# Optimization experiments

Hardware: AMD Instinct MI355X
Metric: run time of the kernel (lower is better)

## Reference

```python
import jax, jax.numpy as jnp
import numpy as np


def setup_inputs() -> dict:
    key = jax.random.key(0)
    k1, k2, k3, k4 = jax.random.split(key, 4)
    return {
        "src_feat1": jax.random.normal(k1, (4, 1024, 64, 64), dtype=jnp.float32),
        "tar_feat1": jax.random.normal(k2, (4, 1024, 64, 64), dtype=jnp.float32),
        "src_feat2": jax.random.normal(k3, (4, 2048, 32, 32), dtype=jnp.float32),
        "tar_feat2": jax.random.normal(k4, (4, 2048, 32, 32), dtype=jnp.float32),
    }


def _nn_concat(src, tar):
    # src: [B,C,H1,W1], tar: [B,C,H2,W2] -> [B,2C,H1,W1]
    B, C, H, W = src.shape
    s = src.reshape(B, C, -1).transpose(0, 2, 1)   # [B,N1,C]
    t = tar.reshape(B, C, -1).transpose(0, 2, 1)   # [B,N2,C]
    # squared euclidean distance (argmin of d^2 == argmin of d, sqrt monotonic)
    d2 = (
        jnp.sum(s * s, axis=-1, keepdims=True)      # [B,N1,1]
        + jnp.sum(t * t, axis=-1)[:, None, :]       # [B,1,N2]
        - 2.0 * jnp.einsum("bnc,bmc->bnm", s, t)    # [B,N1,N2]
    )
    idx = jnp.argmin(d2, axis=2)                    # [B,N1]
    nearest = jnp.take_along_axis(t, idx[..., None], axis=1)  # [B,N1,C]
    nearest = nearest.transpose(0, 2, 1).reshape(B, C, H, W)
    return jnp.concatenate([src, nearest], axis=1)


def reference(src_feat1, tar_feat1, src_feat2, tar_feat2):
    c1 = _nn_concat(src_feat1, tar_feat1)           # [B,2048,64,64]
    c2 = _nn_concat(src_feat2, tar_feat2)           # [B,4096,32,32]
    B, C2 = c2.shape[:2]
    H1, W1 = c1.shape[2], c1.shape[3]
    # F.interpolate(mode='bilinear', align_corners=False) == jax.image.resize 'linear'
    c2r = jax.image.resize(c2, (B, C2, H1, W1), method="linear")
    return jnp.concatenate([c1, c2r], axis=1)       # [B,6144,64,64]
```

## Files before the change

### kernel.cpp

```cpp
#include <hip/hip_runtime.h>
#include <cstdint>

using u8 = unsigned char;
using u64 = unsigned long long;

typedef _Float16 f16x8 __attribute__((ext_vector_type(8)));
typedef float f32x4 __attribute__((ext_vector_type(4)));
typedef unsigned short u16x8 __attribute__((ext_vector_type(8)));

__device__ __forceinline__ void gload16(const void* g, void* l) {
  __builtin_amdgcn_global_load_lds((const __attribute__((address_space(1))) void*)g,
                                   (__attribute__((address_space(3))) void*)l, 16, 0, 0);
}

#define VMCNT(N) asm volatile("s_waitcnt vmcnt(" #N ")" ::: "memory")

template <bool WITH_HN>
__global__ __launch_bounds__(256) void split_convert(const float* __restrict__ in,
                                                     _Float16* __restrict__ hi,
                                                     _Float16* __restrict__ lo,
                                                     float* __restrict__ hnp,
                                                     int C, int N) {
  const int n = blockIdx.y * 256 + threadIdx.x;
  const int c0 = blockIdx.x * 32;
  const int b = blockIdx.z;
  const float* inB = in + (size_t)b * C * N;
  f16x8 hv[4], lv[4];
  float ss = 0.f;
#pragma unroll
  for (int g = 0; g < 4; ++g)
#pragma unroll
    for (int e = 0; e < 8; ++e) {
      float x = inB[(size_t)(c0 + g * 8 + e) * N + n];
      _Float16 h = (_Float16)x;
      float r = (x - (float)h) * 4096.f;
      hv[g][e] = h;
      lv[g][e] = (_Float16)r;
      if (WITH_HN) ss = fmaf(x, x, ss);
    }
  _Float16* oh = hi + ((size_t)b * N + n) * C + c0;
  _Float16* ol = lo + ((size_t)b * N + n) * C + c0;
#pragma unroll
  for (int g = 0; g < 4; ++g) {
    *(f16x8*)(oh + g * 8) = hv[g];
    *(f16x8*)(ol + g * 8) = lv[g];
  }
  if (WITH_HN)
    hnp[((size_t)b * gridDim.x + blockIdx.x) * N + n] = ss;
}

__global__ __launch_bounds__(256) void hn_reduce(const float* __restrict__ hnp,
                                                 float* __restrict__ hn,
                                                 int NC, int N) {
  const int n = blockIdx.x * 256 + threadIdx.x;
  const int b = blockIdx.y;
  float acc = 0.f;
  for (int cc = 0; cc < NC; ++cc) acc += hnp[((size_t)b * NC + cc) * N + n];
  hn[(size_t)b * N + n] = 0.5f * acc;
}

#define MFMA_BLOCK(GI)                                                         \
  __builtin_amdgcn_s_barrier();                                                \
  asm volatile("s_waitcnt lgkmcnt(0)" ::: "memory");                           \
  __builtin_amdgcn_sched_barrier(0);                                           \
  __builtin_amdgcn_s_setprio(1);                                               \
  _Pragma("unroll") for (int i2 = 0; i2 < 4; ++i2)                             \
      _Pragma("unroll") for (int j = 0; j < NJ; ++j) acc[(GI)*4 + i2][j] =     \
      __builtin_amdgcn_mfma_f32_16x16x32_f16(av[i2], bv[j],                    \
                                             acc[(GI)*4 + i2][j], 0, 0, 0);    \
  __builtin_amdgcn_s_setprio(0);                                               \
  asm volatile("" ::: "memory");                                               \
  __builtin_amdgcn_s_barrier();

template <int MI, int NJ, int WCN, int NTH>
__global__ __launch_bounds__(NTH, 2) void nn_filter8(
    const u8* __restrict__ Ahi, const u8* __restrict__ Bhi,
    const float* __restrict__ hn, unsigned short* __restrict__ sc,
    int M, int N, int NT , int mBlocks, int nBlocks) {
  constexpr int BM = 2 * MI * 16;
  constexpr int G = MI / 4;
  constexpr int CHUNK_A = BM * 64;
  constexpr int CHUNK = 2 * CHUNK_A;
  __shared__ u8 smem[4 * CHUNK];

  const int tid = threadIdx.x;
  const int lane = tid & 63;
  const int wid = tid >> 6;
  const int wrow = wid / WCN;
  const int wcol = wid % WCN;
  const int lr = lane & 15, kh = lane >> 4;

  const int cpx = (int)gridDim.x >> 3;
  const int bid = (int)blockIdx.x;
  const int sbid = (bid & 7) * cpx + (bid >> 3);
  const int perB = mBlocks * nBlocks;
  const int b = sbid / perB;
  const int rr = sbid - b * perB;
  const int n1 = rr & 3;
  const int t2 = rr >> 2;
  const int mb = t2 % mBlocks;
  const int n2 = t2 / mBlocks;
  const int mbase = mb * BM;
  const int nbase = (n2 * 4 + n1) * BM;
  const size_t rstride = (size_t)NT * 128;

  const int r0 = (tid >> 6) * 16 + ((tid & 63) >> 2);
  const int sA = ((lane & 3) ^ (r0 >> 1)) & 3;
  const u8* aP0 = Ahi + ((size_t)b * M + mbase + r0) * rstride + sA * 16;
  const u8* aP1 = aP0 + (size_t)(NTH / 4) * rstride;
  const u8* bP0 = Bhi + ((size_t)b * N + nbase + r0) * rstride + sA * 16;
  const u8* bP1 = bP0 + (size_t)(NTH / 4) * rstride;

  auto STAGE = [&](int X, int h) {
    const size_t ko = (size_t)X * 128 + h * 64;
    u8* cb = smem + ((X & 1) * 2 + h) * CHUNK;
    gload16(aP0 + ko, cb + tid * 16);
    gload16(aP1 + ko, cb + NTH * 16 + tid * 16);
    gload16(bP0 + ko, cb + CHUNK_A + tid * 16);
    gload16(bP1 + ko, cb + CHUNK_A + NTH * 16 + tid * 16);
  };

  int a_off[MI], b_off[NJ];
#pragma unroll
  for (int i = 0; i < MI; ++i) {
    const int row = wrow * (MI * 16) + i * 16 + lr;
    a_off[i] = row * 64 + (((kh ^ (row >> 1)) & 3) << 4);
  }
#pragma unroll
  for (int j = 0; j < NJ; ++j) {
    const int row = wcol * (NJ * 16) + j * 16 + lr;
    b_off[j] = CHUNK_A + row * 64 + (((kh ^ (row >> 1)) & 3) << 4);
  }

  f32x4 acc[MI][NJ];
#pragma unroll
  for (int i = 0; i < MI; ++i)
#pragma unroll
    for (int j = 0; j < NJ; ++j) acc[i][j] = f32x4{0.f, 0.f, 0.f, 0.f};

  STAGE(0, 0);
  STAGE(0, 1);
  STAGE(1, 0);
  VMCNT(8);
  __builtin_amdgcn_s_barrier();

  for (int X = 0; X < NT; ++X) {
    const u8* cb0 = smem + ((X & 1) * 2) * CHUNK;
    const u8* cb1 = cb0 + CHUNK;
    f16x8 av[4], bv[NJ];

#pragma unroll
    for (int j = 0; j < NJ; ++j) bv[j] = *(const f16x8*)(cb0 + b_off[j]);
#pragma unroll
    for (int i2 = 0; i2 < 4; ++i2) av[i2] = *(const f16x8*)(cb0 + a_off[i2]);
    if (X + 1 < NT) STAGE(X + 1, 1);
    if (X + 1 < NT) { VMCNT(8); } else { VMCNT(0); }
    MFMA_BLOCK(0)

    if constexpr (G == 2) {
#pragma unroll
      for (int i2 = 0; i2 < 4; ++i2) av[i2] = *(const f16x8*)(cb0 + a_off[4 + i2]);
      MFMA_BLOCK(1)
    }

#pragma unroll
    for (int j = 0; j < NJ; ++j) bv[j] = *(const f16x8*)(cb1 + b_off[j]);
#pragma unroll
    for (int i2 = 0; i2 < 4; ++i2) av[i2] = *(const f16x8*)(cb1 + a_off[i2]);
    if (X + 2 < NT) STAGE(X + 2, 0);
    if (X + 1 < NT) {
      if (X + 2 < NT) { VMCNT(8); } else { VMCNT(4); }
    }
    MFMA_BLOCK(0)

    if constexpr (G == 2) {
#pragma unroll
      for (int i2 = 0; i2 < 4; ++i2) av[i2] = *(const f16x8*)(cb1 + a_off[4 + i2]);
      MFMA_BLOCK(1)
    }
  }

  const float* hnB = hn + (size_t)b * N;
  float hnv[NJ];
  int ncol[NJ];
#pragma unroll
  for (int j = 0; j < NJ; ++j) {
    ncol[j] = nbase + wcol * (NJ * 16) + j * 16 + lr;
    hnv[j] = hnB[ncol[j]];
  }
  unsigned short* scB = sc + (size_t)b * M * N;
#pragma unroll
  for (int i = 0; i < MI; ++i)
#pragma unroll
    for (int r = 0; r < 4; ++r) {
      const int m = mbase + wrow * (MI * 16) + i * 16 + kh * 4 + r;
      unsigned short* srow = scB + (size_t)m * N;
#pragma unroll
      for (int j = 0; j < NJ; ++j) {
        float score = hnv[j] - acc[i][j][r];
        int qi = (int)(score * 64.0f);
        qi = qi < 0 ? 0 : (qi > 65535 ? 65535 : qi);
        srow[ncol[j]] = (unsigned short)qi;
      }
    }
}

template <int K, int CH>
__global__ __launch_bounds__(256) void select_rescore(
    const unsigned short* __restrict__ sc,
    const _Float16* __restrict__ hiA, const _Float16* __restrict__ loA,
    const _Float16* __restrict__ hiB, const _Float16* __restrict__ loB,
    const float* __restrict__ hn, unsigned* __restrict__ idx, int M, int N) {
  const int w = threadIdx.x >> 6, lane = threadIdx.x & 63;
  const int row = blockIdx.x * 4 + w;
  const int b = blockIdx.y;
  const unsigned short* q = sc + ((size_t)b * M + row) * N;

  unsigned cm[CH];
#pragma unroll
  for (int ch = 0; ch < CH; ++ch) {
    u16x8 v = *(const u16x8*)(q + ch * 512 + lane * 8);
    unsigned m0 = v[0] < v[1] ? v[0] : v[1];
    unsigned m1 = v[2] < v[3] ? v[2] : v[3];
    unsigned m2 = v[4] < v[5] ? v[4] : v[5];
    unsigned m3 = v[6] < v[7] ? v[6] : v[7];
    m0 = m0 < m1 ? m0 : m1;
    m2 = m2 < m3 ? m2 : m3;
    unsigned m = m0 < m2 ? m0 : m2;
#pragma unroll
    for (int off = 32; off >= 1; off >>= 1) {
      unsigned o = (unsigned)__shfl_xor((int)m, off);
      m = o < m ? o : m;
    }
    cm[ch] = m;
  }
  unsigned mn = 0xFFFFu;
#pragma unroll
  for (int ch = 0; ch < CH; ++ch) mn = cm[ch] < mn ? cm[ch] : mn;
  const unsigned thr = mn + 64;

  constexpr int PER = K / 64;
  const float inv = 2.44140625e-4f;
  float sv[PER];
  const _Float16* hA = hiA + ((size_t)b * M + row) * K;
  const _Float16* lA = loA + ((size_t)b * M + row) * K;
#pragma unroll
  for (int i = 0; i < PER; ++i)
    sv[i] = fmaf((float)lA[i * 64 + lane], inv, (float)hA[i * 64 + lane]);

  float bestv = 3.4e38f;
  int bestn = 0x7FFFFFFF;
  const float* hnB = hn + (size_t)b * N;
#pragma unroll
  for (int ch = 0; ch < CH; ++ch) {
    if (cm[ch] > thr) continue;
    u16x8 v = *(const u16x8*)(q + ch * 512 + lane * 8);
#pragma unroll
    for (int e = 0; e < 8; ++e) {
      u64 mask = __ballot((unsigned)v[e] <= thr);
      while (mask) {
        int bit = __ffsll((long long)mask) - 1;
        mask &= mask - 1;
        int n = ch * 512 + bit * 8 + e;
        const _Float16* hB = hiB + ((size_t)b * N + n) * K;
        const _Float16* lB = loB + ((size_t)b * N + n) * K;
        float part = 0.f;
#pragma unroll
        for (int i = 0; i < PER; ++i)
          part = fmaf(sv[i], fmaf((float)lB[i * 64 + lane], inv, (float)hB[i * 64 + lane]), part);
#pragma unroll
        for (int off = 32; off >= 1; off >>= 1) part += __shfl_xor(part, off);
        float scf = hnB[n] - part;
        if (scf < bestv || (scf == bestv && n < bestn)) { bestv = scf; bestn = n; }
      }
    }
  }
  if (lane == 0) idx[(size_t)b * M + row] = (unsigned)bestn;
}

__global__ __launch_bounds__(256) void write_c1(const float* __restrict__ src1,
                                                const float* __restrict__ tar1,
                                                const unsigned* __restrict__ idx,
                                                float* __restrict__ out) {
  const int b = blockIdx.y, c = blockIdx.x;
  float* orow = out + ((size_t)b * 6144 + c) * 4096;
  if (c < 1024) {
    const float4* s4 = (const float4*)(src1 + ((size_t)b * 1024 + c) * 4096);
    float4* o4 = (float4*)orow;
#pragma unroll
    for (int i = 0; i < 4; ++i) o4[threadIdx.x + i * 256] = s4[threadIdx.x + i * 256];
  } else {
    const float* trow = tar1 + ((size_t)b * 1024 + (c - 1024)) * 4096;
    const unsigned* ib = idx + (size_t)b * 4096;
    for (int p = threadIdx.x; p < 4096; p += 256) orow[p] = trow[ib[p]];
  }
}

__global__ __launch_bounds__(256) void upsample2(const float* __restrict__ src2,
                                                 const float* __restrict__ tar2,
                                                 const unsigned* __restrict__ idx2,
                                                 float* __restrict__ out) {
  __shared__ float row[1024];
  int b = blockIdx.y, c = blockIdx.x;
  if (c < 2048) {
    const float* in = src2 + ((size_t)b * 2048 + c) * 1024;
    for (int p = threadIdx.x; p < 1024; p += 256) row[p] = in[p];
  } else {
    const float* trow = tar2 + ((size_t)b * 2048 + (c - 2048)) * 1024;
    const unsigned* ib = idx2 + (size_t)b * 1024;
    for (int p = threadIdx.x; p < 1024; p += 256) row[p] = trow[ib[p]];
  }
  __syncthreads();
  float* orow = out + ((size_t)b * 6144 + 2048 + c) * 4096;
  for (int q = threadIdx.x; q < 4096; q += 256) {
    int y = q >> 6, x = q & 63;
    int ky = y >> 1, kx = x >> 1;
    int y0, y1, x0, x1;
    float wy0, wy1, wx0, wx1;
    if (y & 1) { y0 = ky; y1 = (ky + 1 < 32) ? ky + 1 : 31; wy0 = 0.75f; wy1 = 0.25f; }
    else       { y0 = (ky > 0) ? ky - 1 : 0; y1 = ky;       wy0 = 0.25f; wy1 = 0.75f; }
    if (x & 1) { x0 = kx; x1 = (kx + 1 < 32) ? kx + 1 : 31; wx0 = 0.75f; wx1 = 0.25f; }
    else       { x0 = (kx > 0) ? kx - 1 : 0; x1 = kx;       wx0 = 0.25f; wx1 = 0.75f; }
    float v = wy0 * (wx0 * row[y0 * 32 + x0] + wx1 * row[y0 * 32 + x1]) +
              wy1 * (wx0 * row[y1 * 32 + x0] + wx1 * row[y1 * 32 + x1]);
    orow[q] = v;
  }
}

extern "C" void kernel_launch(void* const* d_in, const int* in_sizes, int n_in,
                              void* d_out, int out_size, void* d_ws, size_t ws_size,
                              hipStream_t stream) {
  const float* src1 = (const float*)d_in[0];
  const float* tar1 = (const float*)d_in[1];
  const float* src2 = (const float*)d_in[2];
  const float* tar2 = (const float*)d_in[3];
  float* out = (float*)d_out;

  u8* scratch = (u8*)d_out;
  _Float16* hi1s = (_Float16*)scratch;
  _Float16* lo1s = (_Float16*)(scratch + (32ull << 20));
  _Float16* hi1t = (_Float16*)(scratch + (64ull << 20));
  _Float16* lo1t = (_Float16*)(scratch + (96ull << 20));
  _Float16* hi2s = (_Float16*)(scratch + (128ull << 20));
  _Float16* lo2s = (_Float16*)(scratch + (144ull << 20));
  _Float16* hi2t = (_Float16*)(scratch + (160ull << 20));
  _Float16* lo2t = (_Float16*)(scratch + (176ull << 20));
  unsigned short* sc1 = (unsigned short*)(scratch + (192ull << 20));
  unsigned short* sc2 = (unsigned short*)(scratch + (320ull << 20));
  float* hnp1 = (float*)(scratch + (328ull << 20));
  float* hnp2 = (float*)(scratch + (331ull << 20));

  float* hn1 = (float*)d_ws;
  float* hn2 = hn1 + 4 * 4096;
  unsigned* idx1 = (unsigned*)(hn2 + 4 * 1024);
  unsigned* idx2 = idx1 + 4 * 4096;

  split_convert<false><<<dim3(32, 16, 4), 256, 0, stream>>>(src1, hi1s, lo1s, nullptr, 1024, 4096);
  split_convert<true><<<dim3(32, 16, 4), 256, 0, stream>>>(tar1, hi1t, lo1t, hnp1, 1024, 4096);
  split_convert<false><<<dim3(64, 4, 4), 256, 0, stream>>>(src2, hi2s, lo2s, nullptr, 2048, 1024);
  split_convert<true><<<dim3(64, 4, 4), 256, 0, stream>>>(tar2, hi2t, lo2t, hnp2, 2048, 1024);

  hn_reduce<<<dim3(16, 4), 256, 0, stream>>>(hnp1, hn1, 32, 4096);
  hn_reduce<<<dim3(4, 4), 256, 0, stream>>>(hnp2, hn2, 64, 1024);

  nn_filter8<8, 4, 4, 512><<<1024, 512, 0, stream>>>(
      (const u8*)hi1s, (const u8*)hi1t, hn1, sc1, 4096, 4096, 16, 16, 16);
  nn_filter8<4, 4, 2, 256><<<256, 256, 0, stream>>>(
      (const u8*)hi2s, (const u8*)hi2t, hn2, sc2, 1024, 1024, 32, 8, 8);

  select_rescore<1024, 8><<<dim3(1024, 4), 256, 0, stream>>>(
      sc1, hi1s, lo1s, hi1t, lo1t, hn1, idx1, 4096, 4096);
  select_rescore<2048, 2><<<dim3(256, 4), 256, 0, stream>>>(
      sc2, hi2s, lo2s, hi2t, lo2t, hn2, idx2, 1024, 1024);

  write_c1<<<dim3(2048, 4), 256, 0, stream>>>(src1, tar1, idx1, out);
  upsample2<<<dim3(4096, 4), 256, 0, stream>>>(src2, tar2, idx2, out);
}
```

Before: 570.1 us.

## Use int8 MFMA for nearest-neighbour candidate filtering with wider rescore margin

Adds an int8 quantisation of the source and target features, with a fixed scale of 25.4, inside the split/convert pass. The coarse distance GEMM then runs on the int8 MFMA (16x16x64) instead of fp16, which halves the operand bytes and the number of K tiles. Because int8 scores are coarser, the threshold for candidates that go on to exact fp16 hi/lo rescoring is widened from 64 to 320 or 384 quantised units. The costs are extra int8 writes in the convert kernels and more candidates to rescore. The fixed scale and clamp at ±127 assume roughly unit-variance inputs, so if the margin is too narrow the true nearest neighbour could be filtered out.

After: 608.0 us. +6.7%, slower.

```diff
diff --git a/kernel.cpp b/kernel.cpp
--- a/kernel.cpp
+++ b/kernel.cpp
@@ -6,6 +6,8 @@
 
 typedef _Float16 f16x8 __attribute__((ext_vector_type(8)));
 typedef float f32x4 __attribute__((ext_vector_type(4)));
+typedef int i32x4 __attribute__((ext_vector_type(4)));
+typedef signed char i8x8 __attribute__((ext_vector_type(8)));
 typedef unsigned short u16x8 __attribute__((ext_vector_type(8)));
 
 __device__ __forceinline__ void gload16(const void* g, void* l) {
@@ -14,11 +16,15 @@
 }
 
 #define VMCNT(N) asm volatile("s_waitcnt vmcnt(" #N ")" ::: "memory")
+
+#define QSCALE 25.4f
+#define DEQ2 (0.03937007874f * 0.03937007874f)
 
 template <bool WITH_HN>
 __global__ __launch_bounds__(256) void split_convert(const float* __restrict__ in,
                                                      _Float16* __restrict__ hi,
                                                      _Float16* __restrict__ lo,
+                                                     signed char* __restrict__ q8,
                                                      float* __restrict__ hnp,
                                                      int C, int N) {
   const int n = blockIdx.y * 256 + threadIdx.x;
@@ -26,6 +32,7 @@
   const int b = blockIdx.z;
   const float* inB = in + (size_t)b * C * N;
   f16x8 hv[4], lv[4];
+  i8x8 qv[4];
   float ss = 0.f;
 #pragma unroll
   for (int g = 0; g < 4; ++g)
@@ -36,14 +43,19 @@
       float r = (x - (float)h) * 4096.f;
       hv[g][e] = h;
       lv[g][e] = (_Float16)r;
+      int qi = (int)rintf(x * QSCALE);
+      qi = qi > 127 ? 127 : (qi < -127 ? -127 : qi);
+      qv[g][e] = (signed char)qi;
       if (WITH_HN) ss = fmaf(x, x, ss);
     }
   _Float16* oh = hi + ((size_t)b * N + n) * C + c0;
   _Float16* ol = lo + ((size_t)b * N + n) * C + c0;
+  signed char* oq = q8 + ((size_t)b * N + n) * C + c0;
 #pragma unroll
   for (int g = 0; g < 4; ++g) {
     *(f16x8*)(oh + g * 8) = hv[g];
     *(f16x8*)(ol + g * 8) = lv[g];
+    *(i8x8*)(oq + g * 8) = qv[g];
   }
   if (WITH_HN)
     hnp[((size_t)b * gridDim.x + blockIdx.x) * N + n] = ss;
@@ -66,15 +78,15 @@
   __builtin_amdgcn_s_setprio(1);                                               \
   _Pragma("unroll") for (int i2 = 0; i2 < 4; ++i2)                             \
       _Pragma("unroll") for (int j = 0; j < NJ; ++j) acc[(GI)*4 + i2][j] =     \
-      __builtin_amdgcn_mfma_f32_16x16x32_f16(av[i2], bv[j],                    \
-                                             acc[(GI)*4 + i2][j], 0, 0, 0);    \
+      __builtin_amdgcn_mfma_i32_16x16x64_i8(av[i2], bv[j],                     \
+                                            acc[(GI)*4 + i2][j], 0, 0, 0);     \
   __builtin_amdgcn_s_setprio(0);                                               \
   asm volatile("" ::: "memory");                                               \
   __builtin_amdgcn_s_barrier();
 
 template <int MI, int NJ, int WCN, int NTH>
-__global__ __launch_bounds__(NTH, 2) void nn_filter8(
-    const u8* __restrict__ Ahi, const u8* __restrict__ Bhi,
+__global__ __launch_bounds__(NTH, 2) void nn_filter_i8(
+    const signed char* __restrict__ Aq, const signed char* __restrict__ Bq,
     const float* __restrict__ hn, unsigned short* __restrict__ sc,
     int M, int N, int NT , int mBlocks, int nBlocks) {
   constexpr int BM = 2 * MI * 16;
@@ -106,9 +118,9 @@
 
   const int r0 = (tid >> 6) * 16 + ((tid & 63) >> 2);
   const int sA = ((lane & 3) ^ (r0 >> 1)) & 3;
-  const u8* aP0 = Ahi + ((size_t)b * M + mbase + r0) * rstride + sA * 16;
+  const u8* aP0 = (const u8*)Aq + ((size_t)b * M + mbase + r0) * rstride + sA * 16;
   const u8* aP1 = aP0 + (size_t)(NTH / 4) * rstride;
-  const u8* bP0 = Bhi + ((size_t)b * N + nbase + r0) * rstride + sA * 16;
+  const u8* bP0 = (const u8*)Bq + ((size_t)b * N + nbase + r0) * rstride + sA * 16;
   const u8* bP1 = bP0 + (size_t)(NTH / 4) * rstride;
 
   auto STAGE = [&](int X, int h) {
@@ -132,11 +144,11 @@
     b_off[j] = CHUNK_A + row * 64 + (((kh ^ (row >> 1)) & 3) << 4);
   }
 
-  f32x4 acc[MI][NJ];
+  i32x4 acc[MI][NJ];
 #pragma unroll
   for (int i = 0; i < MI; ++i)
 #pragma unroll
-    for (int j = 0; j < NJ; ++j) acc[i][j] = f32x4{0.f, 0.f, 0.f, 0.f};
+    for (int j = 0; j < NJ; ++j) acc[i][j] = i32x4{0, 0, 0, 0};
 
   STAGE(0, 0);
   STAGE(0, 1);
@@ -147,26 +159,26 @@
   for (int X = 0; X < NT; ++X) {
     const u8* cb0 = smem + ((X & 1) * 2) * CHUNK;
     const u8* cb1 = cb0 + CHUNK;
-    f16x8 av[4], bv[NJ];
-
-#pragma unroll
-    for (int j = 0; j < NJ; ++j) bv[j] = *(const f16x8*)(cb0 + b_off[j]);
-#pragma unroll
-    for (int i2 = 0; i2 < 4; ++i2) av[i2] = *(const f16x8*)(cb0 + a_off[i2]);
+    i32x4 av[4], bv[NJ];
+
+#pragma unroll
+    for (int j = 0; j < NJ; ++j) bv[j] = *(const i32x4*)(cb0 + b_off[j]);
+#pragma unroll
+    for (int i2 = 0; i2 < 4; ++i2) av[i2] = *(const i32x4*)(cb0 + a_off[i2]);
     if (X + 1 < NT) STAGE(X + 1, 1);
     if (X + 1 < NT) { VMCNT(8); } else { VMCNT(0); }
     MFMA_BLOCK(0)
 
     if constexpr (G == 2) {
 #pragma unroll
-      for (int i2 = 0; i2 < 4; ++i2) av[i2] = *(const f16x8*)(cb0 + a_off[4 + i2]);
+      for (int i2 = 0; i2 < 4; ++i2) av[i2] = *(const i32x4*)(cb0 + a_off[4 + i2]);
       MFMA_BLOCK(1)
     }
 
 #pragma unroll
-    for (int j = 0; j < NJ; ++j) bv[j] = *(const f16x8*)(cb1 + b_off[j]);
-#pragma unroll
-    for (int i2 = 0; i2 < 4; ++i2) av[i2] = *(const f16x8*)(cb1 + a_off[i2]);
+    for (int j = 0; j < NJ; ++j) bv[j] = *(const i32x4*)(cb1 + b_off[j]);
+#pragma unroll
+    for (int i2 = 0; i2 < 4; ++i2) av[i2] = *(const i32x4*)(cb1 + a_off[i2]);
     if (X + 2 < NT) STAGE(X + 2, 0);
     if (X + 1 < NT) {
       if (X + 2 < NT) { VMCNT(8); } else { VMCNT(4); }
@@ -175,7 +187,7 @@
 
     if constexpr (G == 2) {
 #pragma unroll
-      for (int i2 = 0; i2 < 4; ++i2) av[i2] = *(const f16x8*)(cb1 + a_off[4 + i2]);
+      for (int i2 = 0; i2 < 4; ++i2) av[i2] = *(const i32x4*)(cb1 + a_off[4 + i2]);
       MFMA_BLOCK(1)
     }
   }
@@ -197,7 +209,7 @@
       unsigned short* srow = scB + (size_t)m * N;
 #pragma unroll
       for (int j = 0; j < NJ; ++j) {
-        float score = hnv[j] - acc[i][j][r];
+        float score = hnv[j] - (float)acc[i][j][r] * DEQ2;
         int qi = (int)(score * 64.0f);
         qi = qi < 0 ? 0 : (qi > 65535 ? 65535 : qi);
         srow[ncol[j]] = (unsigned short)qi;
@@ -210,7 +222,8 @@
     const unsigned short* __restrict__ sc,
     const _Float16* __restrict__ hiA, const _Float16* __restrict__ loA,
     const _Float16* __restrict__ hiB, const _Float16* __restrict__ loB,
-    const float* __restrict__ hn, unsigned* __restrict__ idx, int M, int N) {
+    const float* __restrict__ hn, unsigned* __restrict__ idx,
+    int M, int N, int dq ) {
   const int w = threadIdx.x >> 6, lane = threadIdx.x & 63;
   const int row = blockIdx.x * 4 + w;
   const int b = blockIdx.y;
@@ -237,7 +250,7 @@
   unsigned mn = 0xFFFFu;
 #pragma unroll
   for (int ch = 0; ch < CH; ++ch) mn = cm[ch] < mn ? cm[ch] : mn;
-  const unsigned thr = mn + 64;
+  const unsigned thr = mn + dq;
 
   constexpr int PER = K / 64;
   const float inv = 2.44140625e-4f;
@@ -349,29 +362,33 @@
   unsigned short* sc2 = (unsigned short*)(scratch + (320ull << 20));
   float* hnp1 = (float*)(scratch + (328ull << 20));
   float* hnp2 = (float*)(scratch + (331ull << 20));
+  signed char* q1s = (signed char*)(scratch + (332ull << 20));
+  signed char* q1t = (signed char*)(scratch + (348ull << 20));
+  signed char* q2s = (signed char*)(scratch + (364ull << 20));
+  signed char* q2t = (signed char*)(scratch + (372ull << 20));
 
   float* hn1 = (float*)d_ws;
   float* hn2 = hn1 + 4 * 4096;
   unsigned* idx1 = (unsigned*)(hn2 + 4 * 1024);
   unsigned* idx2 = idx1 + 4 * 4096;
 
-  split_convert<false><<<dim3(32, 16, 4), 256, 0, stream>>>(src1, hi1s, lo1s, nullptr, 1024, 4096);
-  split_convert<true><<<dim3(32, 16, 4), 256, 0, stream>>>(tar1, hi1t, lo1t, hnp1, 1024, 4096);
-  split_convert<false><<<dim3(64, 4, 4), 256, 0, stream>>>(src2, hi2s, lo2s, nullptr, 2048, 1024);
-  split_convert<true><<<dim3(64, 4, 4), 256, 0, stream>>>(tar2, hi2t, lo2t, hnp2, 2048, 1024);
+  split_convert<false><<<dim3(32, 16, 4), 256, 0, stream>>>(src1, hi1s, lo1s, q1s, nullptr, 1024, 4096);
+  split_convert<true><<<dim3(32, 16, 4), 256, 0, stream>>>(tar1, hi1t, lo1t, q1t, hnp1, 1024, 4096);
+  split_convert<false><<<dim3(64, 4, 4), 256, 0, stream>>>(src2, hi2s, lo2s, q2s, nullptr, 2048, 1024);
+  split_convert<true><<<dim3(64, 4, 4), 256, 0, stream>>>(tar2, hi2t, lo2t, q2t, hnp2, 2048, 1024);
 
   hn_reduce<<<dim3(16, 4), 256, 0, stream>>>(hnp1, hn1, 32, 4096);
   hn_reduce<<<dim3(4, 4), 256, 0, stream>>>(hnp2, hn2, 64, 1024);
 
-  nn_filter8<8, 4, 4, 512><<<1024, 512, 0, stream>>>(
-      (const u8*)hi1s, (const u8*)hi1t, hn1, sc1, 4096, 4096, 16, 16, 16);
-  nn_filter8<4, 4, 2, 256><<<256, 256, 0, stream>>>(
-      (const u8*)hi2s, (const u8*)hi2t, hn2, sc2, 1024, 1024, 32, 8, 8);
+  nn_filter_i8<8, 4, 4, 512><<<1024, 512, 0, stream>>>(
+      q1s, q1t, hn1, sc1, 4096, 4096, 8, 16, 16);
+  nn_filter_i8<4, 4, 2, 256><<<256, 256, 0, stream>>>(
+      q2s, q2t, hn2, sc2, 1024, 1024, 16, 8, 8);
 
   select_rescore<1024, 8><<<dim3(1024, 4), 256, 0, stream>>>(
-      sc1, hi1s, lo1s, hi1t, lo1t, hn1, idx1, 4096, 4096);
+      sc1, hi1s, lo1s, hi1t, lo1t, hn1, idx1, 4096, 4096, 320);
   select_rescore<2048, 2><<<dim3(256, 4), 256, 0, stream>>>(
-      sc2, hi2s, lo2s, hi2t, lo2t, hn2, idx2, 1024, 1024);
+      sc2, hi2s, lo2s, hi2t, lo2t, hn2, idx2, 1024, 1024, 384);
 
   write_c1<<<dim3(2048, 4), 256, 0, stream>>>(src1, tar1, idx1, out);
   upsample2<<<dim3(4096, 4), 256, 0, stream>>>(src2, tar2, idx2, out);
```

## Replace full quantized score matrix with per-tile candidate lists in filter epilogue

Applied to the files above, without the earlier changes.

The filter kernel no longer writes the full quantized u16 distance matrix. For each row it now finds the tile minimum through shuffles and shared memory, then keeps only candidates within a threshold of that minimum, capped at 12 per tile, in compact count and entry arrays. The select kernel takes the global minimum from these lists and rescores only the surviving candidates. This removes most of the score-matrix write and read traffic, at the cost of extra epilogue barriers and atomics. Candidates beyond the cap are silently dropped, which could change results when many near-ties occur.

Measured after the change: 591.8 us. 3.8% more time.

```diff
diff --git a/kernel.cpp b/kernel.cpp
--- a/kernel.cpp
+++ b/kernel.cpp
@@ -72,10 +72,14 @@
   asm volatile("" ::: "memory");                                               \
   __builtin_amdgcn_s_barrier();
 
+constexpr int CAP = 12;
+constexpr unsigned DELTA_Q = 64;
+
 template <int MI, int NJ, int WCN, int NTH>
 __global__ __launch_bounds__(NTH, 2) void nn_filter8(
     const u8* __restrict__ Ahi, const u8* __restrict__ Bhi,
-    const float* __restrict__ hn, unsigned short* __restrict__ sc,
+    const float* __restrict__ hn,
+    unsigned* __restrict__ g_cnt, unsigned* __restrict__ g_ent,
     int M, int N, int NT , int mBlocks, int nBlocks) {
   constexpr int BM = 2 * MI * 16;
   constexpr int G = MI / 4;
@@ -101,7 +105,8 @@
   const int mb = t2 % mBlocks;
   const int n2 = t2 / mBlocks;
   const int mbase = mb * BM;
-  const int nbase = (n2 * 4 + n1) * BM;
+  const int tileIdx = n2 * 4 + n1;
+  const int nbase = tileIdx * BM;
   const size_t rstride = (size_t)NT * 128;
 
   const int r0 = (tid >> 6) * 16 + ((tid & 63) >> 2);
@@ -188,56 +193,100 @@
     ncol[j] = nbase + wcol * (NJ * 16) + j * 16 + lr;
     hnv[j] = hnB[ncol[j]];
   }
-  unsigned short* scB = sc + (size_t)b * M * N;
+
+  unsigned* lmin = (unsigned*)smem;
+  unsigned* tmin = (unsigned*)(smem + BM * WCN * 4);
+  unsigned* lcnt = tmin + BM;
+  unsigned* lent = lcnt + BM;
+
+  auto quant = [&](int i, int j, int r) -> unsigned {
+    float s = hnv[j] - acc[i][j][r];
+    int qi = (int)(s * 64.0f);
+    return (unsigned)(qi < 0 ? 0 : (qi > 65535 ? 65535 : qi));
+  };
+
 #pragma unroll
   for (int i = 0; i < MI; ++i)
 #pragma unroll
     for (int r = 0; r < 4; ++r) {
-      const int m = mbase + wrow * (MI * 16) + i * 16 + kh * 4 + r;
-      unsigned short* srow = scB + (size_t)m * N;
+      unsigned rq = 0xFFFFFFFFu;
 #pragma unroll
       for (int j = 0; j < NJ; ++j) {
-        float score = hnv[j] - acc[i][j][r];
-        int qi = (int)(score * 64.0f);
-        qi = qi < 0 ? 0 : (qi > 65535 ? 65535 : qi);
-        srow[ncol[j]] = (unsigned short)qi;
+        unsigned q = quant(i, j, r);
+        rq = q < rq ? q : rq;
       }
-    }
-}
-
-template <int K, int CH>
-__global__ __launch_bounds__(256) void select_rescore(
-    const unsigned short* __restrict__ sc,
+#pragma unroll
+      for (int off = 1; off <= 8; off <<= 1) {
+        unsigned o = (unsigned)__shfl_xor((int)rq, off);
+        rq = o < rq ? o : rq;
+      }
+      if (lr == 0) {
+        const int ml = wrow * (MI * 16) + i * 16 + kh * 4 + r;
+        lmin[ml * WCN + wcol] = rq;
+      }
+    }
+  __syncthreads();
+  for (int m = tid; m < BM; m += NTH) {
+    unsigned t = lmin[m * WCN];
+#pragma unroll
+    for (int w = 1; w < WCN; ++w) {
+      unsigned o = lmin[m * WCN + w];
+      t = o < t ? o : t;
+    }
+    tmin[m] = t;
+    lcnt[m] = 0;
+  }
+  __syncthreads();
+#pragma unroll
+  for (int i = 0; i < MI; ++i)
+#pragma unroll
+    for (int r = 0; r < 4; ++r) {
+      const int ml = wrow * (MI * 16) + i * 16 + kh * 4 + r;
+      const unsigned lim = tmin[ml] + DELTA_Q;
+#pragma unroll
+      for (int j = 0; j < NJ; ++j) {
+        unsigned q = quant(i, j, r);
+        if (q <= lim) {
+          unsigned slot = atomicAdd(&lcnt[ml], 1u);
+          if (slot < CAP) lent[ml * CAP + slot] = (q << 16) | (unsigned)ncol[j];
+        }
+      }
+    }
+  __syncthreads();
+  for (int m = tid; m < BM; m += NTH) {
+    unsigned c = lcnt[m];
+    unsigned cc = c < CAP ? c : CAP;
+    const size_t base = ((size_t)b * M + mbase + m) * nBlocks + tileIdx;
+    g_cnt[base] = cc;
+    for (unsigned e = 0; e < cc; ++e) g_ent[base * CAP + e] = lent[m * CAP + e];
+  }
+}
+
+template <int K, int NTILES>
+__global__ __launch_bounds__(256) void select_cand(
+    const unsigned* __restrict__ g_cnt, const unsigned* __restrict__ g_ent,
     const _Float16* __restrict__ hiA, const _Float16* __restrict__ loA,
     const _Float16* __restrict__ hiB, const _Float16* __restrict__ loB,
     const float* __restrict__ hn, unsigned* __restrict__ idx, int M, int N) {
   const int w = threadIdx.x >> 6, lane = threadIdx.x & 63;
   const int row = blockIdx.x * 4 + w;
   const int b = blockIdx.y;
-  const unsigned short* q = sc + ((size_t)b * M + row) * N;
-
-  unsigned cm[CH];
-#pragma unroll
-  for (int ch = 0; ch < CH; ++ch) {
-    u16x8 v = *(const u16x8*)(q + ch * 512 + lane * 8);
-    unsigned m0 = v[0] < v[1] ? v[0] : v[1];
-    unsigned m1 = v[2] < v[3] ? v[2] : v[3];
-    unsigned m2 = v[4] < v[5] ? v[4] : v[5];
-    unsigned m3 = v[6] < v[7] ? v[6] : v[7];
-    m0 = m0 < m1 ? m0 : m1;
-    m2 = m2 < m3 ? m2 : m3;
-    unsigned m = m0 < m2 ? m0 : m2;
-#pragma unroll
-    for (int off = 32; off >= 1; off >>= 1) {
-      unsigned o = (unsigned)__shfl_xor((int)m, off);
-      m = o < m ? o : m;
-    }
-    cm[ch] = m;
-  }
-  unsigned mn = 0xFFFFu;
-#pragma unroll
-  for (int ch = 0; ch < CH; ++ch) mn = cm[ch] < mn ? cm[ch] : mn;
-  const unsigned thr = mn + 64;
+  const size_t rowbase = ((size_t)b * M + row) * NTILES;
+
+  unsigned key = 0xFFFFFFFFu;
+  if (lane < NTILES) {
+    unsigned c = g_cnt[rowbase + lane];
+    for (unsigned e = 0; e < c; ++e) {
+      unsigned en = g_ent[(rowbase + lane) * CAP + e];
+      key = en < key ? en : key;
+    }
+  }
+#pragma unroll
+  for (int off = 32; off >= 1; off >>= 1) {
+    unsigned o = (unsigned)__shfl_xor((int)key, off);
+    key = o < key ? o : key;
+  }
+  const unsigned thr = (key >> 16) + DELTA_Q;
 
   constexpr int PER = K / 64;
   const float inv = 2.44140625e-4f;
@@ -251,28 +300,22 @@
   float bestv = 3.4e38f;
   int bestn = 0x7FFFFFFF;
   const float* hnB = hn + (size_t)b * N;
-#pragma unroll
-  for (int ch = 0; ch < CH; ++ch) {
-    if (cm[ch] > thr) continue;
-    u16x8 v = *(const u16x8*)(q + ch * 512 + lane * 8);
-#pragma unroll
-    for (int e = 0; e < 8; ++e) {
-      u64 mask = __ballot((unsigned)v[e] <= thr);
-      while (mask) {
-        int bit = __ffsll((long long)mask) - 1;
-        mask &= mask - 1;
-        int n = ch * 512 + bit * 8 + e;
-        const _Float16* hB = hiB + ((size_t)b * N + n) * K;
-        const _Float16* lB = loB + ((size_t)b * N + n) * K;
-        float part = 0.f;
-#pragma unroll
-        for (int i = 0; i < PER; ++i)
-          part = fmaf(sv[i], fmaf((float)lB[i * 64 + lane], inv, (float)hB[i * 64 + lane]), part);
-#pragma unroll
-        for (int off = 32; off >= 1; off >>= 1) part += __shfl_xor(part, off);
-        float scf = hnB[n] - part;
-        if (scf < bestv || (scf == bestv && n < bestn)) { bestv = scf; bestn = n; }
-      }
+  for (int t = 0; t < NTILES; ++t) {
+    unsigned c = g_cnt[rowbase + t];
+    for (unsigned e = 0; e < c; ++e) {
+      unsigned en = g_ent[(rowbase + t) * CAP + e];
+      if ((en >> 16) > thr) continue;
+      int n = (int)(en & 0xFFFFu);
+      const _Float16* hB = hiB + ((size_t)b * N + n) * K;
+      const _Float16* lB = loB + ((size_t)b * N + n) * K;
+      float part = 0.f;
+#pragma unroll
+      for (int i = 0; i < PER; ++i)
+        part = fmaf(sv[i], fmaf((float)lB[i * 64 + lane], inv, (float)hB[i * 64 + lane]), part);
+#pragma unroll
+      for (int off = 32; off >= 1; off >>= 1) part += __shfl_xor(part, off);
+      float scf = hnB[n] - part;
+      if (scf < bestv || (scf == bestv && n < bestn)) { bestv = scf; bestn = n; }
     }
   }
   if (lane == 0) idx[(size_t)b * M + row] = (unsigned)bestn;
@@ -345,10 +388,12 @@
   _Float16* lo2s = (_Float16*)(scratch + (144ull << 20));
   _Float16* hi2t = (_Float16*)(scratch + (160ull << 20));
   _Float16* lo2t = (_Float16*)(scratch + (176ull << 20));
-  unsigned short* sc1 = (unsigned short*)(scratch + (192ull << 20));
-  unsigned short* sc2 = (unsigned short*)(scratch + (320ull << 20));
-  float* hnp1 = (float*)(scratch + (328ull << 20));
-  float* hnp2 = (float*)(scratch + (331ull << 20));
+  float* hnp1 = (float*)(scratch + (192ull << 20));
+  float* hnp2 = (float*)(scratch + (195ull << 20));
+  unsigned* cnt1 = (unsigned*)(scratch + (200ull << 20));
+  unsigned* ent1 = (unsigned*)(scratch + (202ull << 20));
+  unsigned* cnt2 = (unsigned*)(scratch + (216ull << 20));
+  unsigned* ent2 = (unsigned*)(scratch + (218ull << 20));
 
   float* hn1 = (float*)d_ws;
   float* hn2 = hn1 + 4 * 4096;
@@ -364,14 +409,14 @@
   hn_reduce<<<dim3(4, 4), 256, 0, stream>>>(hnp2, hn2, 64, 1024);
 
   nn_filter8<8, 4, 4, 512><<<1024, 512, 0, stream>>>(
-      (const u8*)hi1s, (const u8*)hi1t, hn1, sc1, 4096, 4096, 16, 16, 16);
+      (const u8*)hi1s, (const u8*)hi1t, hn1, cnt1, ent1, 4096, 4096, 16, 16, 16);
   nn_filter8<4, 4, 2, 256><<<256, 256, 0, stream>>>(
-      (const u8*)hi2s, (const u8*)hi2t, hn2, sc2, 1024, 1024, 32, 8, 8);
-
-  select_rescore<1024, 8><<<dim3(1024, 4), 256, 0, stream>>>(
-      sc1, hi1s, lo1s, hi1t, lo1t, hn1, idx1, 4096, 4096);
-  select_rescore<2048, 2><<<dim3(256, 4), 256, 0, stream>>>(
-      sc2, hi2s, lo2s, hi2t, lo2t, hn2, idx2, 1024, 1024);
+      (const u8*)hi2s, (const u8*)hi2t, hn2, cnt2, ent2, 1024, 1024, 32, 8, 8);
+
+  select_cand<1024, 16><<<dim3(1024, 4), 256, 0, stream>>>(
+      cnt1, ent1, hi1s, lo1s, hi1t, lo1t, hn1, idx1, 4096, 4096);
+  select_cand<2048, 8><<<dim3(256, 4), 256, 0, stream>>>(
+      cnt2, ent2, hi2s, lo2s, hi2t, lo2t, hn2, idx2, 1024, 1024);
 
   write_c1<<<dim3(2048, 4), 256, 0, stream>>>(src1, tar1, idx1, out);
   upsample2<<<dim3(4096, 4), 256, 0, stream>>>(src2, tar2, idx2, out);
```
